# Optimization experiments

Measured on AMD Instinct MI355X. Metric: run time of the kernel, lower is better.

The kernel has to match this reference:

```python
import jax, jax.numpy as jnp
import numpy as np

B, T, F, U = 64, 2048, 256, 32


def setup_inputs() -> dict:
    key = jax.random.key(0)
    k0, k1, k2, k3, k4 = jax.random.split(key, 5)
    return {
        "x": jax.random.normal(k0, (B, T, F), jnp.float32),
        "kernel": jax.random.normal(k1, (F, U), jnp.float32) * (1.0 / np.sqrt(F)),
        "bias": jnp.zeros((U,), jnp.float32),
        "chain_kernel": jax.random.normal(k2, (U, U), jnp.float32) * 0.1,
        "left_boundary": jax.random.normal(k3, (U,), jnp.float32) * 0.1,
        "right_boundary": jax.random.normal(k4, (U,), jnp.float32) * 0.1,
    }


def _potentials(x, kernel, bias, left_boundary, right_boundary):
    # Dense (linear activation) + boundary energies at first/last timestep (mask=None path)
    pot = jnp.einsum("btf,fu->btu", x, kernel) + bias
    pot = pot.at[:, 0, :].add(left_boundary)
    pot = pot.at[:, -1, :].add(right_boundary)
    return pot  # [B, T, U]


def _viterbi(pot, chain):
    # pot: [B,T,U], chain: [U,U]; max-plus forward recursion + backtrack
    init = pot[:, 0]  # [B,U]

    def fwd(state, pot_t):
        # scores[b,i,j] = state[b,i] + chain[i,j]
        scores = state[:, :, None] + chain[None]
        bp = jnp.argmax(scores, axis=1).astype(jnp.int32)  # [B,U] backpointers
        new_state = jnp.max(scores, axis=1) + pot_t        # [B,U]
        return new_state, bp

    last, bps = jax.lax.scan(fwd, init, jnp.swapaxes(pot, 0, 1)[1:])  # bps: [T-1,B,U]
    best_score = jnp.max(last, axis=-1)                   # [B]
    last_tag = jnp.argmax(last, axis=-1).astype(jnp.int32)  # [B]

    def back(tag, bp_t):
        prev = jnp.take_along_axis(bp_t, tag[:, None], axis=1)[:, 0]
        return prev, prev

    _, tags_rev = jax.lax.scan(back, last_tag, bps[::-1])  # [T-1,B]
    tags = jnp.concatenate([tags_rev[::-1], last_tag[None]], axis=0)  # [T,B]
    return jnp.swapaxes(tags, 0, 1).astype(jnp.int32), best_score


def reference(x, kernel, bias, chain_kernel, left_boundary, right_boundary):
    pot = _potentials(x, kernel, bias, left_boundary, right_boundary)
    decoded, _ = _viterbi(pot, chain_kernel)
    return decoded  # [B, T] int32
```

## Files before the change

kernel.cpp:

```cpp
#include <hip/hip_runtime.h>
#include <hip/hip_bf16.h>
#include <cstdint>

#define BB 64
#define TT 2048
#define FD 256
#define UU 32

__global__ __launch_bounds__(256, 4) void potentials_kernel(
    const float* __restrict__ x, const float* __restrict__ K,
    const float* __restrict__ bias, const float* __restrict__ lb,
    const float* __restrict__ rb, float* __restrict__ pot)
{
    __shared__ float Kt[UU * 260];

    const int tid = threadIdx.x;
    const int u = tid & 31;
    const int g = tid >> 5;

    for (int idx = tid; idx < FD * UU; idx += 256) {
        const int f = idx >> 5;
        const int uu = idx & 31;
        Kt[uu * 260 + f] = K[idx];
    }
    __syncthreads();

    const float bu = bias[u];
    const float lu = lb[u];
    const float ru = rb[u];

    const int tiles = (BB * TT) / 32;
    for (int tile = blockIdx.x; tile < tiles; tile += gridDim.x) {
        const int row0 = tile * 32;
        const float* x0 = x + (size_t)(row0 + g) * FD;

        float acc0 = 0.f, acc1 = 0.f, acc2 = 0.f, acc3 = 0.f;
        #pragma unroll 4
        for (int f = 0; f < FD; f += 4) {
            const float4 kq = *(const float4*)&Kt[u * 260 + f];
            const float4 xa = *(const float4*)(x0 + f);
            const float4 xb = *(const float4*)(x0 + 8 * FD + f);
            const float4 xc = *(const float4*)(x0 + 16 * FD + f);
            const float4 xd = *(const float4*)(x0 + 24 * FD + f);
            acc0 += xa.x * kq.x; acc0 += xa.y * kq.y; acc0 += xa.z * kq.z; acc0 += xa.w * kq.w;
            acc1 += xb.x * kq.x; acc1 += xb.y * kq.y; acc1 += xb.z * kq.z; acc1 += xb.w * kq.w;
            acc2 += xc.x * kq.x; acc2 += xc.y * kq.y; acc2 += xc.z * kq.z; acc2 += xc.w * kq.w;
            acc3 += xd.x * kq.x; acc3 += xd.y * kq.y; acc3 += xd.z * kq.z; acc3 += xd.w * kq.w;
        }

        const int r0 = row0 + g;
        const int r1 = r0 + 8;
        const int r2 = r0 + 16;
        const int r3 = r0 + 24;
        const int t0 = r0 & (TT - 1), t1 = r1 & (TT - 1);
        const int t2 = r2 & (TT - 1), t3 = r3 & (TT - 1);
        pot[(size_t)r0 * UU + u] = acc0 + bu + (t0 == 0 ? lu : 0.f) + (t0 == TT - 1 ? ru : 0.f);
        pot[(size_t)r1 * UU + u] = acc1 + bu + (t1 == 0 ? lu : 0.f) + (t1 == TT - 1 ? ru : 0.f);
        pot[(size_t)r2 * UU + u] = acc2 + bu + (t2 == 0 ? lu : 0.f) + (t2 == TT - 1 ? ru : 0.f);
        pot[(size_t)r3 * UU + u] = acc3 + bu + (t3 == 0 ? lu : 0.f) + (t3 == TT - 1 ? ru : 0.f);
    }
}

__device__ __forceinline__ float quad_swap(float v) {
    const int i = __float_as_int(v);
    const int r = __builtin_amdgcn_update_dpp(i, i, 0xB1, 0xF, 0xF, true);
    return __int_as_float(r);
}

__global__ __launch_bounds__(64) void vit_values_kernel(
    const float* __restrict__ pot, const float* __restrict__ chain,
    float* __restrict__ chk)
{
    __shared__ __align__(16) float mbuf[32];

    const int lane = threadIdx.x;
    const int u = lane >> 1;
    const int q = lane & 1;
    const int qb = 16 * q;
    const int b = blockIdx.x;
    const float* pb = pot + (size_t)b * TT * UU;

    float cc[16];
    #pragma unroll
    for (int i = 0; i < 16; ++i) cc[i] = chain[(qb + i) * UU + u];

    float s[16];
    {
        const float4* s0 = (const float4*)(pb + qb);
        #pragma unroll
        for (int k = 0; k < 4; ++k) {
            const float4 v = s0[k];
            s[4*k+0] = v.x; s[4*k+1] = v.y; s[4*k+2] = v.z; s[4*k+3] = v.w;
        }
    }

    auto step = [&](float potv, int t) {
        float a[16];
        #pragma unroll
        for (int i = 0; i < 16; ++i) a[i] = s[i] + cc[i];
        float m8[8];
        #pragma unroll
        for (int i = 0; i < 8; ++i) m8[i] = fmaxf(a[2*i], a[2*i+1]);
        float m4[4];
        #pragma unroll
        for (int i = 0; i < 4; ++i) m4[i] = fmaxf(m8[2*i], m8[2*i+1]);
        const float pm = fmaxf(fmaxf(m4[0], m4[1]), fmaxf(m4[2], m4[3]));
        const float om = quad_swap(pm);
        const float mm = fmaxf(pm, om) + potv;

        mbuf[u] = mm;

        if ((t & 63) == 63)
            chk[((size_t)b * 33 + ((t >> 6) + 1)) * UU + u] = mm;

        const float4 x0 = *(const float4*)&mbuf[qb + 0];
        const float4 x1 = *(const float4*)&mbuf[qb + 4];
        const float4 x2 = *(const float4*)&mbuf[qb + 8];
        const float4 x3 = *(const float4*)&mbuf[qb + 12];
        s[0]=x0.x;  s[1]=x0.y;  s[2]=x0.z;  s[3]=x0.w;
        s[4]=x1.x;  s[5]=x1.y;  s[6]=x1.z;  s[7]=x1.w;
        s[8]=x2.x;  s[9]=x2.y;  s[10]=x2.z; s[11]=x2.w;
        s[12]=x3.x; s[13]=x3.y; s[14]=x3.z; s[15]=x3.w;
    };

    float pr[8], pn[8];
    #pragma unroll
    for (int j = 0; j < 8; ++j) pr[j] = pb[(1 + j) * UU + u];

    #pragma unroll 1
    for (int g = 0; g < 255; ++g) {
        #pragma unroll
        for (int j = 0; j < 8; ++j) {
            int tp = 9 + 8 * g + j;
            if (tp > TT - 1) tp = TT - 1;
            pn[j] = pb[tp * UU + u];
        }
        const int t0 = 1 + 8 * g;
        #pragma unroll
        for (int j = 0; j < 8; ++j)
            step(pr[j], t0 + j);
        #pragma unroll
        for (int j = 0; j < 8; ++j) pr[j] = pn[j];
    }
    #pragma unroll
    for (int j = 0; j < 7; ++j)
        step(pr[j], 2041 + j);
}

__global__ __launch_bounds__(64) void vit_window_kernel(
    const float* __restrict__ pot, const float* __restrict__ chain,
    const float* __restrict__ chk, unsigned char* __restrict__ Mg,
    unsigned char* __restrict__ bpg)
{
    __shared__ float potL[64 * 32];
    __shared__ float mbuf[32];

    const int lane = threadIdx.x;
    const int u = lane & 31;
    const int h = lane >> 5;
    const int hbase = 16 * h;
    const int w = blockIdx.x;
    const int b = blockIdx.y;
    const float* pb = pot + (size_t)b * TT * UU;
    const int r0 = 64 * w;

    {
        const float4* src = (const float4*)(pb + (size_t)r0 * UU);
        float4* dst = (float4*)potL;
        #pragma unroll
        for (int k = 0; k < 8; ++k) dst[lane + 64 * k] = src[lane + 64 * k];
    }
    __syncthreads();

    float cc[16];
    #pragma unroll
    for (int i = 0; i < 16; ++i) cc[i] = chain[(hbase + i) * UU + u];

    float s[16];
    if (w == 0) {
        #pragma unroll
        for (int i = 0; i < 16; ++i) s[i] = potL[hbase + i];
    } else {
        #pragma unroll
        for (int i = 0; i < 16; ++i) s[i] = chk[((size_t)b * 33 + w) * UU + hbase + i];
    }

    int orig = u;
    unsigned char* bb = bpg + (size_t)b * (TT - 1) * UU;

    const int tl0 = (w == 0) ? 1 : 0;
    #pragma unroll 1
    for (int tl = tl0; tl < 64; ++tl) {
        const int t = r0 + tl;
        const float potv = potL[tl * UU + u];

        float a[16];
        #pragma unroll
        for (int i = 0; i < 16; ++i) a[i] = s[i] + cc[i];

        float v8[8]; int i8[8];
        #pragma unroll
        for (int i = 0; i < 8; ++i) {
            const bool c = a[2*i+1] > a[2*i];
            v8[i] = c ? a[2*i+1] : a[2*i];
            i8[i] = c ? (2*i+1) : (2*i);
        }
        float v4[4]; int i4[4];
        #pragma unroll
        for (int i = 0; i < 4; ++i) {
            const bool c = v8[2*i+1] > v8[2*i];
            v4[i] = c ? v8[2*i+1] : v8[2*i];
            i4[i] = c ? i8[2*i+1] : i8[2*i];
        }
        float v2[2]; int i2[2];
        #pragma unroll
        for (int i = 0; i < 2; ++i) {
            const bool c = v4[2*i+1] > v4[2*i];
            v2[i] = c ? v4[2*i+1] : v4[2*i];
            i2[i] = c ? i4[2*i+1] : i4[2*i];
        }
        const bool cf = v2[1] > v2[0];
        const float pv = cf ? v2[1] : v2[0];
        const int pidx = hbase + (cf ? i2[1] : i2[0]);

        const float opv = __shfl_xor(pv, 32, 64);
        const int   opi = __shfl_xor(pidx, 32, 64);
        const bool take = h ? (opv >= pv) : (opv > pv);
        const int  mv   = take ? opi : pidx;
        const float mm  = fmaxf(pv, opv) + potv;

        if (h == 0) bb[(size_t)(t - 1) * UU + u] = (unsigned char)mv;
        orig = __shfl(orig, mv, 64);

        mbuf[u] = mm;
        const float4 x0 = *(const float4*)&mbuf[hbase + 0];
        const float4 x1 = *(const float4*)&mbuf[hbase + 4];
        const float4 x2 = *(const float4*)&mbuf[hbase + 8];
        const float4 x3 = *(const float4*)&mbuf[hbase + 12];
        s[0]=x0.x; s[1]=x0.y; s[2]=x0.z;  s[3]=x0.w;
        s[4]=x1.x; s[5]=x1.y; s[6]=x1.z;  s[7]=x1.w;
        s[8]=x2.x; s[9]=x2.y; s[10]=x2.z; s[11]=x2.w;
        s[12]=x3.x; s[13]=x3.y; s[14]=x3.z; s[15]=x3.w;
    }

    if (h == 0) Mg[(size_t)b * 1024 + w * UU + u] = (unsigned char)orig;
}

__global__ __launch_bounds__(64) void vit_backtrack_kernel(
    const float* __restrict__ chk, const unsigned char* __restrict__ Mg,
    const unsigned char* __restrict__ bpg, int* __restrict__ out)
{
    __shared__ unsigned char Ml[1024];
    __shared__ int tagw[32];

    const int lane = threadIdx.x;
    const int b = blockIdx.x;

    ((int4*)Ml)[lane] = ((const int4*)(Mg + (size_t)b * 1024))[lane];

    float fv = (lane < 32) ? chk[((size_t)b * 33 + 32) * UU + lane] : -INFINITY;
    int fi = lane & 31;
    #pragma unroll
    for (int mask = 16; mask >= 1; mask >>= 1) {
        const float ov = __shfl_xor(fv, mask, 64);
        const int oi = __shfl_xor(fi, mask, 64);
        if (ov > fv || (ov == fv && oi < fi)) { fv = ov; fi = oi; }
    }
    int bt = __shfl(fi, 0, 64);

    __syncthreads();
    #pragma unroll 1
    for (int w = 31; w >= 0; --w) {
        if (lane == 0) tagw[w] = bt;
        bt = Ml[w * 32 + bt];
    }
    __syncthreads();

    if (lane < 32) {
        const int w = lane;
        int tag = tagw[w];
        int t = w * 64 + 63;
        int* ob = out + (size_t)b * TT;
        const unsigned char* bb = bpg + (size_t)b * (TT - 1) * UU;
        ob[t] = tag;
        #pragma unroll 1
        for (; t >= w * 64 + 1; --t) {
            tag = bb[(size_t)(t - 1) * UU + tag];
            ob[t - 1] = tag;
        }
    }
}

extern "C" void kernel_launch(void* const* d_in, const int* in_sizes, int n_in,
                              void* d_out, int out_size, void* d_ws, size_t ws_size,
                              hipStream_t stream)
{
    const float* x     = (const float*)d_in[0];
    const float* K     = (const float*)d_in[1];
    const float* bias  = (const float*)d_in[2];
    const float* chain = (const float*)d_in[3];
    const float* lb    = (const float*)d_in[4];
    const float* rb    = (const float*)d_in[5];
    int* out = (int*)d_out;

    float* pot = (float*)d_ws;
    float* chk = pot + (size_t)BB * TT * UU;
    unsigned char* Mg  = (unsigned char*)(chk + (size_t)BB * 33 * UU);
    unsigned char* bpg = Mg + (size_t)BB * 32 * UU;

    potentials_kernel<<<1024, 256, 0, stream>>>(x, K, bias, lb, rb, pot);
    vit_values_kernel<<<BB, 64, 0, stream>>>(pot, chain, chk);
    vit_window_kernel<<<dim3(32, BB), 64, 0, stream>>>(pot, chain, chk, Mg, bpg);
    vit_backtrack_kernel<<<BB, 64, 0, stream>>>(chk, Mg, bpg, out);
}
```

Before: 562.3 us.

## Register-tile potentials GEMM via swizzled LDS and stage backpointers in LDS for backtrack

The potentials kernel now stages a 32-row tile of x into XOR-swizzled shared memory. Each thread computes a 4x4 register tile of outputs, with 512 single-wavefront blocks in place of 256-thread blocks that read x directly from global memory. The backtrack kernel copies the whole per-batch backpointer table (about 64KB) into LDS so the serial per-window chase hits shared memory instead of global bytes. It also reads the window map straight from global memory and keeps each window's start tag in a register. The trade-offs are far fewer threads for the GEMM, fewer resident blocks because of large LDS use, and an added bulk copy before backtracking.

```diff
diff --git a/kernel.cpp b/kernel.cpp
--- a/kernel.cpp
+++ b/kernel.cpp
@@ -7,57 +7,82 @@
 #define FD 256
 #define UU 32
 
-__global__ __launch_bounds__(256, 4) void potentials_kernel(
+__global__ __launch_bounds__(64) void potentials_kernel(
     const float* __restrict__ x, const float* __restrict__ K,
     const float* __restrict__ bias, const float* __restrict__ lb,
     const float* __restrict__ rb, float* __restrict__ pot)
 {
-    __shared__ float Kt[UU * 260];
+    __shared__ __align__(16) float lds[16384];
+    float* xs = lds;
+    float* Kt = lds + 8192;
 
     const int tid = threadIdx.x;
-    const int u = tid & 31;
-    const int g = tid >> 5;
-
-    for (int idx = tid; idx < FD * UU; idx += 256) {
-        const int f = idx >> 5;
-        const int uu = idx & 31;
-        Kt[uu * 260 + f] = K[idx];
-    }
-    __syncthreads();
-
-    const float bu = bias[u];
-    const float lu = lb[u];
-    const float ru = rb[u];
+    const int ug = tid & 7;
+    const int rg = tid >> 3;
+
+    for (int j = 0; j < 128; ++j) {
+        const int e = j * 64 + tid;
+        const int f = e >> 5;
+        const int u = e & 31;
+        Kt[u * 256 + (((f >> 2) ^ (u & 7)) << 2) + (f & 3)] = K[e];
+    }
+
+    float bu[4], lu4[4], ru4[4];
+    #pragma unroll
+    for (int m = 0; m < 4; ++m) {
+        bu[m]  = bias[ug + 8 * m];
+        lu4[m] = lb[ug + 8 * m];
+        ru4[m] = rb[ug + 8 * m];
+    }
 
     const int tiles = (BB * TT) / 32;
     for (int tile = blockIdx.x; tile < tiles; tile += gridDim.x) {
         const int row0 = tile * 32;
-        const float* x0 = x + (size_t)(row0 + g) * FD;
-
-        float acc0 = 0.f, acc1 = 0.f, acc2 = 0.f, acc3 = 0.f;
+        __syncthreads();
         #pragma unroll 4
-        for (int f = 0; f < FD; f += 4) {
-            const float4 kq = *(const float4*)&Kt[u * 260 + f];
-            const float4 xa = *(const float4*)(x0 + f);
-            const float4 xb = *(const float4*)(x0 + 8 * FD + f);
-            const float4 xc = *(const float4*)(x0 + 16 * FD + f);
-            const float4 xd = *(const float4*)(x0 + 24 * FD + f);
-            acc0 += xa.x * kq.x; acc0 += xa.y * kq.y; acc0 += xa.z * kq.z; acc0 += xa.w * kq.w;
-            acc1 += xb.x * kq.x; acc1 += xb.y * kq.y; acc1 += xb.z * kq.z; acc1 += xb.w * kq.w;
-            acc2 += xc.x * kq.x; acc2 += xc.y * kq.y; acc2 += xc.z * kq.z; acc2 += xc.w * kq.w;
-            acc3 += xd.x * kq.x; acc3 += xd.y * kq.y; acc3 += xd.z * kq.z; acc3 += xd.w * kq.w;
-        }
-
-        const int r0 = row0 + g;
-        const int r1 = r0 + 8;
-        const int r2 = r0 + 16;
-        const int r3 = r0 + 24;
-        const int t0 = r0 & (TT - 1), t1 = r1 & (TT - 1);
-        const int t2 = r2 & (TT - 1), t3 = r3 & (TT - 1);
-        pot[(size_t)r0 * UU + u] = acc0 + bu + (t0 == 0 ? lu : 0.f) + (t0 == TT - 1 ? ru : 0.f);
-        pot[(size_t)r1 * UU + u] = acc1 + bu + (t1 == 0 ? lu : 0.f) + (t1 == TT - 1 ? ru : 0.f);
-        pot[(size_t)r2 * UU + u] = acc2 + bu + (t2 == 0 ? lu : 0.f) + (t2 == TT - 1 ? ru : 0.f);
-        pot[(size_t)r3 * UU + u] = acc3 + bu + (t3 == 0 ? lu : 0.f) + (t3 == TT - 1 ? ru : 0.f);
+        for (int k = 0; k < 32; ++k) {
+            const float4 v = *(const float4*)(x + (size_t)(row0 + k) * FD + tid * 4);
+            *(float4*)&xs[k * 256 + ((tid ^ (k & 7)) << 2)] = v;
+        }
+        __syncthreads();
+
+        float acc[4][4];
+        #pragma unroll
+        for (int i = 0; i < 4; ++i)
+            #pragma unroll
+            for (int m = 0; m < 4; ++m) acc[i][m] = 0.f;
+
+        #pragma unroll 4
+        for (int q = 0; q < 64; ++q) {
+            float4 xq[4], kq[4];
+            #pragma unroll
+            for (int i = 0; i < 4; ++i)
+                xq[i] = *(const float4*)&xs[(rg + 8 * i) * 256 + ((q ^ rg) << 2)];
+            #pragma unroll
+            for (int m = 0; m < 4; ++m)
+                kq[m] = *(const float4*)&Kt[(ug + 8 * m) * 256 + ((q ^ ug) << 2)];
+            #pragma unroll
+            for (int i = 0; i < 4; ++i)
+                #pragma unroll
+                for (int m = 0; m < 4; ++m) {
+                    acc[i][m] += xq[i].x * kq[m].x;
+                    acc[i][m] += xq[i].y * kq[m].y;
+                    acc[i][m] += xq[i].z * kq[m].z;
+                    acc[i][m] += xq[i].w * kq[m].w;
+                }
+        }
+
+        #pragma unroll
+        for (int i = 0; i < 4; ++i) {
+            const int row = row0 + rg + 8 * i;
+            const int t = row & (TT - 1);
+            #pragma unroll
+            for (int m = 0; m < 4; ++m) {
+                pot[(size_t)row * UU + ug + 8 * m] =
+                    acc[i][m] + bu[m] + (t == 0 ? lu4[m] : 0.f)
+                              + (t == TT - 1 ? ru4[m] : 0.f);
+            }
+        }
     }
 }
 
@@ -250,13 +275,18 @@
     const float* __restrict__ chk, const unsigned char* __restrict__ Mg,
     const unsigned char* __restrict__ bpg, int* __restrict__ out)
 {
-    __shared__ unsigned char Ml[1024];
-    __shared__ int tagw[32];
+    __shared__ __align__(16) unsigned char bp[(TT - 1) * UU];
 
     const int lane = threadIdx.x;
     const int b = blockIdx.x;
-
-    ((int4*)Ml)[lane] = ((const int4*)(Mg + (size_t)b * 1024))[lane];
+    const unsigned char* bb = bpg + (size_t)b * (TT - 1) * UU;
+
+    #pragma unroll 4
+    for (int i = 0; i < 64; ++i) {
+        const int idx = i * 64 + lane;
+        if (idx < 4094)
+            ((int4*)bp)[idx] = ((const int4*)bb)[idx];
+    }
 
     float fv = (lane < 32) ? chk[((size_t)b * 33 + 32) * UU + lane] : -INFINITY;
     int fi = lane & 31;
@@ -268,24 +298,24 @@
     }
     int bt = __shfl(fi, 0, 64);
 
-    __syncthreads();
+    int my_btag = 0;
     #pragma unroll 1
     for (int w = 31; w >= 0; --w) {
-        if (lane == 0) tagw[w] = bt;
-        bt = Ml[w * 32 + bt];
-    }
+        if (lane == w) my_btag = bt;
+        bt = Mg[(size_t)b * 1024 + w * 32 + bt];
+    }
+
     __syncthreads();
 
     if (lane < 32) {
         const int w = lane;
-        int tag = tagw[w];
+        int tag = my_btag;
         int t = w * 64 + 63;
         int* ob = out + (size_t)b * TT;
-        const unsigned char* bb = bpg + (size_t)b * (TT - 1) * UU;
         ob[t] = tag;
         #pragma unroll 1
         for (; t >= w * 64 + 1; --t) {
-            tag = bb[(size_t)(t - 1) * UU + tag];
+            tag = bp[(t - 1) * UU + tag];
             ob[t - 1] = tag;
         }
     }
@@ -308,7 +338,7 @@
     unsigned char* Mg  = (unsigned char*)(chk + (size_t)BB * 33 * UU);
     unsigned char* bpg = Mg + (size_t)BB * 32 * UU;
 
-    potentials_kernel<<<1024, 256, 0, stream>>>(x, K, bias, lb, rb, pot);
+    potentials_kernel<<<512, 64, 0, stream>>>(x, K, bias, lb, rb, pot);
     vit_values_kernel<<<BB, 64, 0, stream>>>(pot, chain, chk);
     vit_window_kernel<<<dim3(32, BB), 64, 0, stream>>>(pot, chain, chk, Mg, bpg);
     vit_backtrack_kernel<<<BB, 64, 0, stream>>>(chk, Mg, bpg, out);
```

After: 532.1 us. 1.06x faster.
